# Performance work log

Hardware: AMD Instinct MI355X
Metric: run time of the kernel (lower is better)

The kernel has to match this reference:

```python
import jax, jax.numpy as jnp
import numpy as np

K = 7          # window kernel size
PAD = 3        # padding so out spatial == in spatial (stride=1, dilation=1)
BN_EPS = 1e-5


def conv1x1(x, w, b):
    # x: (b,c,h,w), w: (o,c), b: (o,)
    return jnp.einsum('bchw,oc->bohw', x, w) + b[None, :, None, None]


def bn_relu(x, bn):
    # bn: (4, C) rows = gamma, beta, running_mean, running_var (inference-mode BN)
    g, bta, m, v = bn[0], bn[1], bn[2], bn[3]
    scale = g / jnp.sqrt(v + BN_EPS)
    y = (x - m[None, :, None, None]) * scale[None, :, None, None] + bta[None, :, None, None]
    return jax.nn.relu(y)


def extract_patches(x):
    # Equivalent of F.unfold(x, K, padding=PAD, stride=1) reshaped to (b, C, K*K, H, W).
    # Ordering matches torch: channel major, kernel positions row-major.
    b, c, h, w = x.shape
    xp = jnp.pad(x, ((0, 0), (0, 0), (PAD, PAD), (PAD, PAD)))
    ps = [xp[:, :, i:i + h, j:j + w] for i in range(K) for j in range(K)]
    return jnp.stack(ps, axis=2)  # (b, c, K*K, h, w)


def setup_inputs() -> dict:
    key = jax.random.key(0)
    ks = jax.random.split(key, 20)
    Cin, Ck, Cv, Co = 256, 64, 128, 256
    b, h, w = 2, 96, 96

    def wgt(k, o, c):
        return jax.random.normal(k, (o, c), jnp.float32) * 0.05

    def bias(k, o):
        return jax.random.normal(k, (o,), jnp.float32) * 0.02

    def bn(k, c):
        g = 1.0 + 0.1 * jax.random.normal(k, (c,), jnp.float32)
        bta = 0.1 * jax.random.normal(jax.random.fold_in(k, 1), (c,), jnp.float32)
        m = 0.05 * jax.random.normal(jax.random.fold_in(k, 2), (c,), jnp.float32)
        v = 1.0 + 0.1 * jax.random.uniform(jax.random.fold_in(k, 3), (c,), jnp.float32)
        return jnp.stack([g, bta, m, v])  # (4, c)

    return {
        'x': jax.random.normal(ks[0], (b, Cin, h, w), jnp.float32),
        'fk_w1': wgt(ks[1], Ck, Cin), 'fk_b1': bias(ks[2], Ck), 'fk_bn1': bn(ks[3], Ck),
        'fk_w2': wgt(ks[4], Ck, Ck), 'fk_b2': bias(ks[5], Ck), 'fk_bn2': bn(ks[6], Ck),
        'fq_w1': wgt(ks[7], Ck, Cin), 'fq_b1': bias(ks[8], Ck), 'fq_bn1': bn(ks[9], Ck),
        'fq_w2': wgt(ks[10], Ck, Ck), 'fq_b2': bias(ks[11], Ck), 'fq_bn2': bn(ks[12], Ck),
        'fv_w': wgt(ks[13], Cv, Cin), 'fv_b': bias(ks[14], Cv),
        'W_w': wgt(ks[15], Co, Cv), 'W_b': bias(ks[16], Co),
    }


def reference(x, fk_w1, fk_b1, fk_bn1, fk_w2, fk_b2, fk_bn2,
              fq_w1, fq_b1, fq_bn1, fq_w2, fq_b2, fq_bn2,
              fv_w, fv_b, W_w, W_b):
    # scale=1 -> no pooling. stride=1, dilation=1, pad=3, k=7 -> out spatial == in spatial.
    value = conv1x1(x, fv_w, fv_b)                       # (b, Cv, H, W)
    unfold_value = extract_patches(value)                # (b, Cv, 49, H, W)

    k1 = bn_relu(conv1x1(x, fk_w1, fk_b1), fk_bn1)
    key = bn_relu(conv1x1(k1, fk_w2, fk_b2), fk_bn2)     # (b, Ck, H, W)
    unfold_key = extract_patches(key)                    # (b, Ck, 49, H, W)

    q1 = bn_relu(conv1x1(x, fq_w1, fq_b1), fq_bn1)
    query = bn_relu(conv1x1(q1, fq_w2, fq_b2), fq_bn2)   # (b, Ck, H, W)
    # start_index = dilation*(k//2) - padding = 0; stride=1 -> query slice is identity.

    sim = jnp.sum(unfold_key * query[:, :, None], axis=1, keepdims=True)  # (b,1,49,H,W)
    sim = jax.nn.softmax(sim, axis=2)
    context = jnp.sum(sim * unfold_value, axis=2)        # (b, Cv, H, W)
    context = conv1x1(context, W_w, W_b)                 # (b, Co, H, W)
    # F.interpolate to (h, w) with align_corners=True is identity (same size).
    return context
```

## Files before the change

kernel.cpp:

```cpp
#include <hip/hip_runtime.h>
#include <hip/hip_bf16.h>

typedef _Float16 f16;
typedef _Float16 f16x8 __attribute__((ext_vector_type(8)));
typedef float f32x4 __attribute__((ext_vector_type(4)));

#define HH 96
#define WW 96
#define HWs 9216
#define BN_EPS 1e-5f

#define OFF_XT   0u
#define OFF_ACT1 9437184u
#define OFF_ACT2 18874368u
#define OFF_CTX  23592960u
#define OFF_W1   28311552u
#define OFF_W2   28442624u
#define OFF_W3   28459008u
#define OFF_ST   28524544u

__global__ __launch_bounds__(256) void prep_kernel(
    const float* __restrict__ fk_w1, const float* __restrict__ fk_b1, const float* __restrict__ fk_bn1,
    const float* __restrict__ fk_w2, const float* __restrict__ fk_b2, const float* __restrict__ fk_bn2,
    const float* __restrict__ fq_w1, const float* __restrict__ fq_b1, const float* __restrict__ fq_bn1,
    const float* __restrict__ fq_w2, const float* __restrict__ fq_b2, const float* __restrict__ fq_bn2,
    const float* __restrict__ fv_w,  const float* __restrict__ fv_b,
    const float* __restrict__ W_w,   const float* __restrict__ W_b,
    char* __restrict__ wsb)
{
  f16* w1 = (f16*)(wsb + OFF_W1);
  f16* w2 = (f16*)(wsb + OFF_W2);
  f16* w3 = (f16*)(wsb + OFF_W3);
  float* st = (float*)(wsb + OFF_ST);
  int i = blockIdx.x * 256 + threadIdx.x;
  if (i < 65536) {
    int o = i >> 8, c = i & 255;
    float v;
    if (o < 128)      v = fv_w[o * 256 + c];
    else if (o < 192) v = fk_w1[(o - 128) * 256 + c];
    else              v = fq_w1[(o - 192) * 256 + c];
    w1[i] = (f16)v;
  } else if (i < 73728) {
    int j = i - 65536; int o = j >> 6, c = j & 63;
    w2[j] = (f16)((o < 64) ? fk_w2[o * 64 + c] : fq_w2[(o - 64) * 64 + c]);
  } else if (i < 106496) {
    int j = i - 73728;
    w3[j] = (f16)W_w[j];
  } else if (i < 106752) {
    int o = i - 106496;
    float s, t;
    if (o < 128) { s = 1.0f; t = fv_b[o]; }
    else if (o < 192) {
      int j = o - 128;
      float g = fk_bn1[j], be = fk_bn1[64 + j], m = fk_bn1[128 + j], v = fk_bn1[192 + j];
      s = g * rsqrtf(v + BN_EPS); t = (fk_b1[j] - m) * s + be;
    } else {
      int j = o - 192;
      float g = fq_bn1[j], be = fq_bn1[64 + j], m = fq_bn1[128 + j], v = fq_bn1[192 + j];
      s = g * rsqrtf(v + BN_EPS); t = (fq_b1[j] - m) * s + be;
    }
    st[o] = s; st[256 + o] = t;
  } else if (i < 106880) {
    int o = i - 106752;
    float s, t;
    if (o < 64) {
      float g = fk_bn2[o], be = fk_bn2[64 + o], m = fk_bn2[128 + o], v = fk_bn2[192 + o];
      s = g * rsqrtf(v + BN_EPS); t = (fk_b2[o] - m) * s + be;
    } else {
      int j = o - 64;
      float g = fq_bn2[j], be = fq_bn2[64 + j], m = fq_bn2[128 + j], v = fq_bn2[192 + j];
      s = g * rsqrtf(v + BN_EPS); t = (fq_b2[j] - m) * s + be;
    }
    st[512 + o] = s; st[640 + o] = t;
  } else if (i < 107136) {
    int o = i - 106880;
    st[768 + o] = W_b[o];
  }
}

__global__ __launch_bounds__(256) void transpose_in(const float* __restrict__ x, f16* __restrict__ xT)
{
  __shared__ float lds[64 * 65];
  const int t = threadIdx.x;
  const int p0 = blockIdx.x * 64, c0 = blockIdx.y * 64, bb = blockIdx.z;
#pragma unroll
  for (int pass = 0; pass < 16; ++pass) {
    int ch = pass * 4 + (t >> 6), px = t & 63;
    lds[ch * 65 + px] = x[((size_t)bb * 256 + c0 + ch) * HWs + p0 + px];
  }
  __syncthreads();
#pragma unroll
  for (int pass = 0; pass < 2; ++pass) {
    int pl = pass * 32 + (t >> 3), cs = t & 7;
    f16x8 v;
#pragma unroll
    for (int j = 0; j < 8; j++) v[j] = (f16)lds[(cs * 8 + j) * 65 + pl];
    *(f16x8*)&xT[((size_t)bb * HWs + p0 + pl) * 256 + c0 + cs * 8] = v;
  }
}

template<int KTOT, bool NCHW_OUT>
__global__ __launch_bounds__(256) void gemm128(
    const f16* __restrict__ Aact, int lda, int ka0,
    const f16* __restrict__ W,
    f16* __restrict__ Cout, int ldc, int cbase,
    float* __restrict__ out_nchw,
    const float* __restrict__ S, const float* __restrict__ T, int relu_start)
{
  __shared__ f16 As[128 * 40];
  __shared__ f16 Bs[128 * 40];
  const int tid = threadIdx.x;
  const int l = tid & 63, w = tid >> 6;
  const int bb = blockIdx.z;
  const int p0 = blockIdx.x * 128, n0 = blockIdx.y * 128;
  const f16* Ab = Aact + (size_t)bb * HWs * lda;
  f32x4 acc[4][4];
#pragma unroll
  for (int i = 0; i < 4; i++)
#pragma unroll
    for (int j = 0; j < 4; j++) acc[i][j] = (f32x4){0.f, 0.f, 0.f, 0.f};
  const int wm = (w >> 1) * 64, wn = (w & 1) * 64;
  const int lrow = l & 15, lk = (l >> 4) * 8;
#pragma unroll 1
  for (int ks = 0; ks < KTOT / 32; ks++) {
#pragma unroll
    for (int it = 0; it < 2; it++) {
      int tt = it * 256 + tid;
      int row = tt >> 2, seg = tt & 3;
      *(f16x8*)&As[row * 40 + seg * 8] =
          *(const f16x8*)&Ab[(size_t)(p0 + row) * lda + ka0 + ks * 32 + seg * 8];
      *(f16x8*)&Bs[row * 40 + seg * 8] =
          *(const f16x8*)&W[(size_t)(n0 + row) * KTOT + ks * 32 + seg * 8];
    }
    __syncthreads();
    f16x8 a[4], b[4];
#pragma unroll
    for (int mi = 0; mi < 4; mi++) a[mi] = *(const f16x8*)&As[(wm + mi * 16 + lrow) * 40 + lk];
#pragma unroll
    for (int ni = 0; ni < 4; ni++) b[ni] = *(const f16x8*)&Bs[(wn + ni * 16 + lrow) * 40 + lk];
#pragma unroll
    for (int mi = 0; mi < 4; mi++)
#pragma unroll
      for (int ni = 0; ni < 4; ni++)
        acc[mi][ni] = __builtin_amdgcn_mfma_f32_16x16x32_f16(a[mi], b[ni], acc[mi][ni], 0, 0, 0);
    __syncthreads();
  }
#pragma unroll
  for (int mi = 0; mi < 4; mi++)
#pragma unroll
    for (int ni = 0; ni < 4; ni++) {
      int coutl = n0 + wn + ni * 16 + lrow;
      int pb = p0 + wm + mi * 16 + (l >> 4) * 4;
      if (NCHW_OUT) {
        float t = T[coutl];
        float4 o;
        o.x = acc[mi][ni][0] + t; o.y = acc[mi][ni][1] + t;
        o.z = acc[mi][ni][2] + t; o.w = acc[mi][ni][3] + t;
        *(float4*)&out_nchw[((size_t)bb * 256 + coutl) * HWs + pb] = o;
      } else {
        float s = S[coutl], t = T[coutl];
        bool rl = coutl >= relu_start;
#pragma unroll
        for (int r = 0; r < 4; r++) {
          float v = acc[mi][ni][r] * s + t;
          if (rl) v = fmaxf(v, 0.f);
          Cout[((size_t)bb * HWs + pb + r) * ldc + cbase + coutl] = (f16)v;
        }
      }
    }
}

__global__ __launch_bounds__(256) void gemm_s2(
    const f16* __restrict__ Aact, int ka0,
    const f16* __restrict__ W,
    f16* __restrict__ Cout, int cbase,
    const float* __restrict__ S, const float* __restrict__ T)
{
  __shared__ f16 As[256 * 40];
  __shared__ f16 Bs[64 * 40];
  const int tid = threadIdx.x;
  const int l = tid & 63, w = tid >> 6;
  const int bb = blockIdx.z;
  const int p0 = blockIdx.x * 256;
  const f16* Ab = Aact + (size_t)bb * HWs * 256;
  f32x4 acc[4][4];
#pragma unroll
  for (int i = 0; i < 4; i++)
#pragma unroll
    for (int j = 0; j < 4; j++) acc[i][j] = (f32x4){0.f, 0.f, 0.f, 0.f};
  const int wm = w * 64;
  const int lrow = l & 15, lk = (l >> 4) * 8;
#pragma unroll 1
  for (int ks = 0; ks < 2; ks++) {
#pragma unroll
    for (int it = 0; it < 4; it++) {
      int tt = it * 256 + tid;
      int row = tt >> 2, seg = tt & 3;
      *(f16x8*)&As[row * 40 + seg * 8] =
          *(const f16x8*)&Ab[(size_t)(p0 + row) * 256 + ka0 + ks * 32 + seg * 8];
    }
    {
      int row = tid >> 2, seg = tid & 3;
      *(f16x8*)&Bs[row * 40 + seg * 8] =
          *(const f16x8*)&W[(size_t)row * 64 + ks * 32 + seg * 8];
    }
    __syncthreads();
    f16x8 a[4], b[4];
#pragma unroll
    for (int mi = 0; mi < 4; mi++) a[mi] = *(const f16x8*)&As[(wm + mi * 16 + lrow) * 40 + lk];
#pragma unroll
    for (int ni = 0; ni < 4; ni++) b[ni] = *(const f16x8*)&Bs[(ni * 16 + lrow) * 40 + lk];
#pragma unroll
    for (int mi = 0; mi < 4; mi++)
#pragma unroll
      for (int ni = 0; ni < 4; ni++)
        acc[mi][ni] = __builtin_amdgcn_mfma_f32_16x16x32_f16(a[mi], b[ni], acc[mi][ni], 0, 0, 0);
    __syncthreads();
  }
#pragma unroll
  for (int mi = 0; mi < 4; mi++)
#pragma unroll
    for (int ni = 0; ni < 4; ni++) {
      int coutl = ni * 16 + lrow;
      int pb = p0 + wm + mi * 16 + (l >> 4) * 4;
      float s = S[coutl], t = T[coutl];
#pragma unroll
      for (int r = 0; r < 4; r++) {
        float v = fmaxf(acc[mi][ni][r] * s + t, 0.f);
        Cout[((size_t)bb * HWs + pb + r) * 128 + cbase + coutl] = (f16)v;
      }
    }
}

__global__ __launch_bounds__(256) void attn_kernel(const f16* __restrict__ act1,
                                                   const f16* __restrict__ act2,
                                                   f16* __restrict__ ctx)
{
  __shared__ float Ps[64 * 52];
  __shared__ f16 buf[208 * 136];
  const int tid = threadIdx.x;
  const int l = tid & 63, w = tid >> 6;
  const int bb = blockIdx.z;
  const int x0 = blockIdx.x * 8, y0 = blockIdx.y * 8;
  const f16* a2 = act2 + (size_t)bb * HWs * 128;
  const f16* a1 = act1 + (size_t)bb * HWs * 256;
  f16* ctxb = ctx + (size_t)bb * HWs * 128;
  f16* Qs = buf;
  f16* Ks = buf + 64 * 72;

#pragma unroll
  for (int it = 0; it < 2; it++) {
    int t = it * 256 + tid;
    int q = t >> 3, seg = t & 7;
    int gp = (y0 + (q >> 3)) * WW + x0 + (q & 7);
    *(f16x8*)&Qs[q * 72 + seg * 8] = *(const f16x8*)&a2[(size_t)gp * 128 + 64 + seg * 8];
  }
  for (int t = tid; t < 1664; t += 256) {
    int kk = t >> 3, seg = t & 7;
    int ky = (kk * 4682) >> 16, kx = kk - 14 * ky;
    int gy = y0 - 3 + ky, gx = x0 - 3 + kx;
    f16x8 v = {(f16)0, (f16)0, (f16)0, (f16)0, (f16)0, (f16)0, (f16)0, (f16)0};
    if (kk < 196 && (unsigned)gy < (unsigned)HH && (unsigned)gx < (unsigned)WW)
      v = *(const f16x8*)&a2[((size_t)(gy * WW + gx)) * 128 + seg * 8];
    *(f16x8*)&Ks[kk * 72 + seg * 8] = v;
  }
  __syncthreads();

  f32x4 sc[13];
#pragma unroll
  for (int nj = 0; nj < 13; nj++) sc[nj] = (f32x4){0.f, 0.f, 0.f, 0.f};
  const int lrow = l & 15, lk = (l >> 4) * 8;
#pragma unroll
  for (int ks = 0; ks < 2; ks++) {
    f16x8 aq = *(const f16x8*)&Qs[(w * 16 + lrow) * 72 + ks * 32 + lk];
#pragma unroll
    for (int nj = 0; nj < 13; nj++) {
      f16x8 bk = *(const f16x8*)&Ks[(nj * 16 + lrow) * 72 + ks * 32 + lk];
      sc[nj] = __builtin_amdgcn_mfma_f32_16x16x32_f16(aq, bk, sc[nj], 0, 0, 0);
    }
  }
  const int r0 = w * 16 + (l >> 4) * 4;
#pragma unroll
  for (int nj = 0; nj < 13; nj++) {
    int c = nj * 16 + lrow;
    int ky = (c * 4682) >> 16, kx = c - 14 * ky;
#pragma unroll
    for (int r = 0; r < 4; r++) {
      int qy = (r0 + r) >> 3, qx = (r0 + r) & 7;
      bool valid = ((unsigned)(ky - qy) < 7u) && ((unsigned)(kx - qx) < 7u);
      if (!valid) sc[nj][r] = -1e30f;
    }
  }
  float mx[4], sm[4], inv[4];
#pragma unroll
  for (int r = 0; r < 4; r++) {
    mx[r] = -1e30f;
#pragma unroll
    for (int nj = 0; nj < 13; nj++) mx[r] = fmaxf(mx[r], sc[nj][r]);
  }
#pragma unroll
  for (int off = 1; off < 16; off <<= 1)
#pragma unroll
    for (int r = 0; r < 4; r++) mx[r] = fmaxf(mx[r], __shfl_xor(mx[r], off));
#pragma unroll
  for (int r = 0; r < 4; r++) sm[r] = 0.f;
#pragma unroll
  for (int nj = 0; nj < 13; nj++)
#pragma unroll
    for (int r = 0; r < 4; r++) {
      float e = __expf(sc[nj][r] - mx[r]);
      sc[nj][r] = e; sm[r] += e;
    }
#pragma unroll
  for (int off = 1; off < 16; off <<= 1)
#pragma unroll
    for (int r = 0; r < 4; r++) sm[r] += __shfl_xor(sm[r], off);
#pragma unroll
  for (int r = 0; r < 4; r++) inv[r] = 1.0f / sm[r];
#pragma unroll
  for (int nj = 0; nj < 13; nj++) {
    int c = nj * 16 + lrow;
    int ky = (c * 4682) >> 16, kx = c - 14 * ky;
#pragma unroll
    for (int r = 0; r < 4; r++) {
      int qy = (r0 + r) >> 3, qx = (r0 + r) & 7;
      int dy = ky - qy, dx = kx - qx;
      if (((unsigned)dy < 7u) && ((unsigned)dx < 7u))
        Ps[(r0 + r) * 52 + dy * 7 + dx] = sc[nj][r] * inv[r];
    }
  }
  __syncthreads();

  f16* Vs = buf;
  for (int t = tid; t < 3328; t += 256) {
    int kk = t >> 4, seg = t & 15;
    int ky = (kk * 4682) >> 16, kx = kk - 14 * ky;
    int gy = y0 - 3 + ky, gx = x0 - 3 + kx;
    f16x8 v = {(f16)0, (f16)0, (f16)0, (f16)0, (f16)0, (f16)0, (f16)0, (f16)0};
    if (kk < 196 && (unsigned)gy < (unsigned)HH && (unsigned)gx < (unsigned)WW)
      v = *(const f16x8*)&a1[((size_t)(gy * WW + gx)) * 256 + seg * 8];
    *(f16x8*)&Vs[kk * 136 + seg * 8] = v;
  }
  __syncthreads();

  const int q = tid >> 2;
  const int qy = q >> 3, qx = q & 7;
  const int ch0 = (tid & 3) * 32;
  float acc[32];
#pragma unroll
  for (int i = 0; i < 32; i++) acc[i] = 0.f;
#pragma unroll
  for (int dy = 0; dy < 7; dy++)
#pragma unroll
    for (int dx = 0; dx < 7; dx++) {
      float p = Ps[q * 52 + dy * 7 + dx];
      int kk = (qy + dy) * 14 + qx + dx;
      const f16* vp = &Vs[kk * 136 + ch0];
#pragma unroll
      for (int s = 0; s < 4; s++) {
        f16x8 v = *(const f16x8*)&vp[s * 8];
#pragma unroll
        for (int j = 0; j < 8; j++) acc[s * 8 + j] += (float)v[j] * p;
      }
    }
  int gp = (y0 + qy) * WW + x0 + qx;
#pragma unroll
  for (int s = 0; s < 4; s++) {
    f16x8 o;
#pragma unroll
    for (int j = 0; j < 8; j++) o[j] = (f16)acc[s * 8 + j];
    *(f16x8*)&ctxb[(size_t)gp * 128 + ch0 + s * 8] = o;
  }
}

extern "C" void kernel_launch(void* const* d_in, const int* in_sizes, int n_in,
                              void* d_out, int out_size, void* d_ws, size_t ws_size,
                              hipStream_t stream) {
  (void)in_sizes; (void)n_in; (void)out_size; (void)ws_size;
  const float* x      = (const float*)d_in[0];
  const float* fk_w1  = (const float*)d_in[1];
  const float* fk_b1  = (const float*)d_in[2];
  const float* fk_bn1 = (const float*)d_in[3];
  const float* fk_w2  = (const float*)d_in[4];
  const float* fk_b2  = (const float*)d_in[5];
  const float* fk_bn2 = (const float*)d_in[6];
  const float* fq_w1  = (const float*)d_in[7];
  const float* fq_b1  = (const float*)d_in[8];
  const float* fq_bn1 = (const float*)d_in[9];
  const float* fq_w2  = (const float*)d_in[10];
  const float* fq_b2  = (const float*)d_in[11];
  const float* fq_bn2 = (const float*)d_in[12];
  const float* fv_w   = (const float*)d_in[13];
  const float* fv_b   = (const float*)d_in[14];
  const float* W_w    = (const float*)d_in[15];
  const float* W_b    = (const float*)d_in[16];
  char* wsb = (char*)d_ws;
  float* out = (float*)d_out;

  f16* xT   = (f16*)(wsb + OFF_XT);
  f16* act1 = (f16*)(wsb + OFF_ACT1);
  f16* act2 = (f16*)(wsb + OFF_ACT2);
  f16* ctx  = (f16*)(wsb + OFF_CTX);
  f16* w1   = (f16*)(wsb + OFF_W1);
  f16* w2   = (f16*)(wsb + OFF_W2);
  f16* w3   = (f16*)(wsb + OFF_W3);
  float* st = (float*)(wsb + OFF_ST);

  prep_kernel<<<dim3(419), dim3(256), 0, stream>>>(
      fk_w1, fk_b1, fk_bn1, fk_w2, fk_b2, fk_bn2,
      fq_w1, fq_b1, fq_bn1, fq_w2, fq_b2, fq_bn2, fv_w, fv_b, W_w, W_b, wsb);

  transpose_in<<<dim3(144, 4, 2), dim3(256), 0, stream>>>(x, xT);

  gemm128<256, false><<<dim3(72, 2, 2), dim3(256), 0, stream>>>(
      xT, 256, 0, w1, act1, 256, 0, nullptr, st, st + 256, 128);

  gemm_s2<<<dim3(36, 1, 2), dim3(256), 0, stream>>>(
      act1, 128, w2, act2, 0, st + 512, st + 640);
  gemm_s2<<<dim3(36, 1, 2), dim3(256), 0, stream>>>(
      act1, 192, w2 + 64 * 64, act2, 64, st + 512 + 64, st + 640 + 64);

  attn_kernel<<<dim3(12, 12, 2), dim3(256), 0, stream>>>(act1, act2, ctx);

  gemm128<128, true><<<dim3(72, 2, 2), dim3(256), 0, stream>>>(
      ctx, 128, 0, w3, nullptr, 0, 0, out, st, st + 768, 1 << 30);
}
```

Before: 158.3 us.

## Fuse input transpose and conv stages, and fold final 1x1 conv into attention

The separate transpose, first-stage GEMM and two second-stage GEMMs are merged into one conv12 kernel. It reads fp32 NCHW input directly, keeps key/query intermediates in shared memory and applies the second 1x1 conv per 32-pixel tile. The attention kernel now also runs the output projection from a shared-memory context tile and writes NCHW output, removing the ctx buffer round trip and four launches. The trade-offs are smaller GEMM tiles with W1 reloaded per block, strided uncoalesced x reads, and scattered 4-byte output stores.

Result: faster. 138.9 us, median of 2 (-12.2%).

```diff
diff --git a/kernel.cpp b/kernel.cpp
--- a/kernel.cpp
+++ b/kernel.cpp
@@ -2,6 +2,7 @@
 #include <hip/hip_bf16.h>
 
 typedef _Float16 f16;
+typedef _Float16 f16x4 __attribute__((ext_vector_type(4)));
 typedef _Float16 f16x8 __attribute__((ext_vector_type(8)));
 typedef float f32x4 __attribute__((ext_vector_type(4)));
 
@@ -10,14 +11,12 @@
 #define HWs 9216
 #define BN_EPS 1e-5f
 
-#define OFF_XT   0u
-#define OFF_ACT1 9437184u
-#define OFF_ACT2 18874368u
-#define OFF_CTX  23592960u
-#define OFF_W1   28311552u
-#define OFF_W2   28442624u
-#define OFF_W3   28459008u
-#define OFF_ST   28524544u
+#define OFF_ACT1 0u
+#define OFF_ACT2 4718592u
+#define OFF_W1   9437184u
+#define OFF_W2   9568256u
+#define OFF_W3   9584640u
+#define OFF_ST   9650176u
 
 __global__ __launch_bounds__(256) void prep_kernel(
     const float* __restrict__ fk_w1, const float* __restrict__ fk_b1, const float* __restrict__ fk_bn1,
@@ -78,163 +77,115 @@
   }
 }
 
-__global__ __launch_bounds__(256) void transpose_in(const float* __restrict__ x, f16* __restrict__ xT)
+__global__ __launch_bounds__(256) void conv12(
+    const float* __restrict__ x, const f16* __restrict__ W1, const f16* __restrict__ W2,
+    f16* __restrict__ act1, f16* __restrict__ act2, const float* __restrict__ st)
 {
-  __shared__ float lds[64 * 65];
-  const int t = threadIdx.x;
-  const int p0 = blockIdx.x * 64, c0 = blockIdx.y * 64, bb = blockIdx.z;
-#pragma unroll
-  for (int pass = 0; pass < 16; ++pass) {
-    int ch = pass * 4 + (t >> 6), px = t & 63;
-    lds[ch * 65 + px] = x[((size_t)bb * 256 + c0 + ch) * HWs + p0 + px];
-  }
-  __syncthreads();
-#pragma unroll
-  for (int pass = 0; pass < 2; ++pass) {
-    int pl = pass * 32 + (t >> 3), cs = t & 7;
-    f16x8 v;
-#pragma unroll
-    for (int j = 0; j < 8; j++) v[j] = (f16)lds[(cs * 8 + j) * 65 + pl];
-    *(f16x8*)&xT[((size_t)bb * HWs + p0 + pl) * 256 + c0 + cs * 8] = v;
-  }
-}
-
-template<int KTOT, bool NCHW_OUT>
-__global__ __launch_bounds__(256) void gemm128(
-    const f16* __restrict__ Aact, int lda, int ka0,
-    const f16* __restrict__ W,
-    f16* __restrict__ Cout, int ldc, int cbase,
-    float* __restrict__ out_nchw,
-    const float* __restrict__ S, const float* __restrict__ T, int relu_start)
-{
-  __shared__ f16 As[128 * 40];
-  __shared__ f16 Bs[128 * 40];
+  __shared__ f16 As[32 * 40];
+  __shared__ f16 Bs[256 * 40];
+  __shared__ f16 kqs[2][32 * 72];
   const int tid = threadIdx.x;
   const int l = tid & 63, w = tid >> 6;
-  const int bb = blockIdx.z;
-  const int p0 = blockIdx.x * 128, n0 = blockIdx.y * 128;
-  const f16* Ab = Aact + (size_t)bb * HWs * lda;
-  f32x4 acc[4][4];
-#pragma unroll
-  for (int i = 0; i < 4; i++)
+  const int bb = blockIdx.y;
+  const int p0 = blockIdx.x * 32;
+  const int lrow = l & 15, lk = (l >> 4) * 8;
+
+  f32x4 acc[2][4];
+#pragma unroll
+  for (int i = 0; i < 2; i++)
 #pragma unroll
     for (int j = 0; j < 4; j++) acc[i][j] = (f32x4){0.f, 0.f, 0.f, 0.f};
-  const int wm = (w >> 1) * 64, wn = (w & 1) * 64;
-  const int lrow = l & 15, lk = (l >> 4) * 8;
+
+  const int spx = tid & 31, skg = tid >> 5;
 #pragma unroll 1
-  for (int ks = 0; ks < KTOT / 32; ks++) {
-#pragma unroll
-    for (int it = 0; it < 2; it++) {
-      int tt = it * 256 + tid;
-      int row = tt >> 2, seg = tt & 3;
-      *(f16x8*)&As[row * 40 + seg * 8] =
-          *(const f16x8*)&Ab[(size_t)(p0 + row) * lda + ka0 + ks * 32 + seg * 8];
-      *(f16x8*)&Bs[row * 40 + seg * 8] =
-          *(const f16x8*)&W[(size_t)(n0 + row) * KTOT + ks * 32 + seg * 8];
-    }
-    __syncthreads();
-    f16x8 a[4], b[4];
-#pragma unroll
-    for (int mi = 0; mi < 4; mi++) a[mi] = *(const f16x8*)&As[(wm + mi * 16 + lrow) * 40 + lk];
-#pragma unroll
-    for (int ni = 0; ni < 4; ni++) b[ni] = *(const f16x8*)&Bs[(wn + ni * 16 + lrow) * 40 + lk];
-#pragma unroll
-    for (int mi = 0; mi < 4; mi++)
-#pragma unroll
-      for (int ni = 0; ni < 4; ni++)
-        acc[mi][ni] = __builtin_amdgcn_mfma_f32_16x16x32_f16(a[mi], b[ni], acc[mi][ni], 0, 0, 0);
-    __syncthreads();
-  }
-#pragma unroll
-  for (int mi = 0; mi < 4; mi++)
-#pragma unroll
-    for (int ni = 0; ni < 4; ni++) {
-      int coutl = n0 + wn + ni * 16 + lrow;
-      int pb = p0 + wm + mi * 16 + (l >> 4) * 4;
-      if (NCHW_OUT) {
-        float t = T[coutl];
-        float4 o;
-        o.x = acc[mi][ni][0] + t; o.y = acc[mi][ni][1] + t;
-        o.z = acc[mi][ni][2] + t; o.w = acc[mi][ni][3] + t;
-        *(float4*)&out_nchw[((size_t)bb * 256 + coutl) * HWs + pb] = o;
-      } else {
-        float s = S[coutl], t = T[coutl];
-        bool rl = coutl >= relu_start;
-#pragma unroll
-        for (int r = 0; r < 4; r++) {
-          float v = acc[mi][ni][r] * s + t;
-          if (rl) v = fmaxf(v, 0.f);
-          Cout[((size_t)bb * HWs + pb + r) * ldc + cbase + coutl] = (f16)v;
-        }
-      }
-    }
-}
-
-__global__ __launch_bounds__(256) void gemm_s2(
-    const f16* __restrict__ Aact, int ka0,
-    const f16* __restrict__ W,
-    f16* __restrict__ Cout, int cbase,
-    const float* __restrict__ S, const float* __restrict__ T)
-{
-  __shared__ f16 As[256 * 40];
-  __shared__ f16 Bs[64 * 40];
-  const int tid = threadIdx.x;
-  const int l = tid & 63, w = tid >> 6;
-  const int bb = blockIdx.z;
-  const int p0 = blockIdx.x * 256;
-  const f16* Ab = Aact + (size_t)bb * HWs * 256;
-  f32x4 acc[4][4];
-#pragma unroll
-  for (int i = 0; i < 4; i++)
-#pragma unroll
-    for (int j = 0; j < 4; j++) acc[i][j] = (f32x4){0.f, 0.f, 0.f, 0.f};
-  const int wm = w * 64;
-  const int lrow = l & 15, lk = (l >> 4) * 8;
-#pragma unroll 1
-  for (int ks = 0; ks < 2; ks++) {
+  for (int ks = 0; ks < 8; ks++) {
+    f16x4 av;
+#pragma unroll
+    for (int j = 0; j < 4; j++)
+      av[j] = (f16)x[((size_t)bb * 256 + ks * 32 + skg * 4 + j) * HWs + p0 + spx];
+    *(f16x4*)&As[spx * 40 + skg * 4] = av;
 #pragma unroll
     for (int it = 0; it < 4; it++) {
       int tt = it * 256 + tid;
       int row = tt >> 2, seg = tt & 3;
-      *(f16x8*)&As[row * 40 + seg * 8] =
-          *(const f16x8*)&Ab[(size_t)(p0 + row) * 256 + ka0 + ks * 32 + seg * 8];
-    }
-    {
-      int row = tid >> 2, seg = tid & 3;
       *(f16x8*)&Bs[row * 40 + seg * 8] =
-          *(const f16x8*)&W[(size_t)row * 64 + ks * 32 + seg * 8];
+          *(const f16x8*)&W1[(size_t)row * 256 + ks * 32 + seg * 8];
     }
     __syncthreads();
-    f16x8 a[4], b[4];
-#pragma unroll
-    for (int mi = 0; mi < 4; mi++) a[mi] = *(const f16x8*)&As[(wm + mi * 16 + lrow) * 40 + lk];
-#pragma unroll
-    for (int ni = 0; ni < 4; ni++) b[ni] = *(const f16x8*)&Bs[(ni * 16 + lrow) * 40 + lk];
-#pragma unroll
-    for (int mi = 0; mi < 4; mi++)
-#pragma unroll
-      for (int ni = 0; ni < 4; ni++)
-        acc[mi][ni] = __builtin_amdgcn_mfma_f32_16x16x32_f16(a[mi], b[ni], acc[mi][ni], 0, 0, 0);
+    f16x8 a[2], b[4];
+#pragma unroll
+    for (int mi = 0; mi < 2; mi++) a[mi] = *(const f16x8*)&As[(mi * 16 + lrow) * 40 + lk];
+#pragma unroll
+    for (int nj = 0; nj < 4; nj++) b[nj] = *(const f16x8*)&Bs[(w * 64 + nj * 16 + lrow) * 40 + lk];
+#pragma unroll
+    for (int mi = 0; mi < 2; mi++)
+#pragma unroll
+      for (int nj = 0; nj < 4; nj++)
+        acc[mi][nj] = __builtin_amdgcn_mfma_f32_16x16x32_f16(a[mi], b[nj], acc[mi][nj], 0, 0, 0);
     __syncthreads();
   }
-#pragma unroll
-  for (int mi = 0; mi < 4; mi++)
-#pragma unroll
-    for (int ni = 0; ni < 4; ni++) {
-      int coutl = ni * 16 + lrow;
-      int pb = p0 + wm + mi * 16 + (l >> 4) * 4;
-      float s = S[coutl], t = T[coutl];
+
+#pragma unroll
+  for (int mi = 0; mi < 2; mi++)
+#pragma unroll
+    for (int nj = 0; nj < 4; nj++) {
+      int cout = w * 64 + nj * 16 + lrow;
+      float s = st[cout], t = st[256 + cout];
 #pragma unroll
       for (int r = 0; r < 4; r++) {
-        float v = fmaxf(acc[mi][ni][r] * s + t, 0.f);
-        Cout[((size_t)bb * HWs + pb + r) * 128 + cbase + coutl] = (f16)v;
+        int px = mi * 16 + (l >> 4) * 4 + r;
+        float v = acc[mi][nj][r] * s + t;
+        if (w < 2) {
+          act1[((size_t)bb * HWs + p0 + px) * 128 + cout] = (f16)v;
+        } else {
+          kqs[w - 2][px * 72 + (nj * 16 + lrow)] = (f16)fmaxf(v, 0.f);
+        }
       }
     }
+  __syncthreads();
+
+  const int sel = w >> 1, half = w & 1;
+  const f16* W2s = W2 + sel * 64 * 64;
+  f32x4 acc2[2][2];
+#pragma unroll
+  for (int i = 0; i < 2; i++)
+#pragma unroll
+    for (int j = 0; j < 2; j++) acc2[i][j] = (f32x4){0.f, 0.f, 0.f, 0.f};
+#pragma unroll
+  for (int ks = 0; ks < 2; ks++) {
+    f16x8 a2[2], b2[2];
+#pragma unroll
+    for (int mi = 0; mi < 2; mi++)
+      a2[mi] = *(const f16x8*)&kqs[sel][(mi * 16 + lrow) * 72 + ks * 32 + lk];
+#pragma unroll
+    for (int nj = 0; nj < 2; nj++)
+      b2[nj] = *(const f16x8*)&W2s[(size_t)(half * 32 + nj * 16 + lrow) * 64 + ks * 32 + lk];
+#pragma unroll
+    for (int mi = 0; mi < 2; mi++)
+#pragma unroll
+      for (int nj = 0; nj < 2; nj++)
+        acc2[mi][nj] = __builtin_amdgcn_mfma_f32_16x16x32_f16(a2[mi], b2[nj], acc2[mi][nj], 0, 0, 0);
+  }
+#pragma unroll
+  for (int mi = 0; mi < 2; mi++)
+#pragma unroll
+    for (int nj = 0; nj < 2; nj++) {
+      int c2 = sel * 64 + half * 32 + nj * 16 + lrow;
+      float s = st[512 + c2], t = st[640 + c2];
+#pragma unroll
+      for (int r = 0; r < 4; r++) {
+        int px = mi * 16 + (l >> 4) * 4 + r;
+        float v = fmaxf(acc2[mi][nj][r] * s + t, 0.f);
+        act2[((size_t)bb * HWs + p0 + px) * 128 + c2] = (f16)v;
+      }
+    }
 }
 
-__global__ __launch_bounds__(256) void attn_kernel(const f16* __restrict__ act1,
-                                                   const f16* __restrict__ act2,
-                                                   f16* __restrict__ ctx)
+__global__ __launch_bounds__(256) void attn_final(const f16* __restrict__ act1,
+                                                  const f16* __restrict__ act2,
+                                                  const f16* __restrict__ W3,
+                                                  const float* __restrict__ st,
+                                                  float* __restrict__ out)
 {
   __shared__ float Ps[64 * 52];
   __shared__ f16 buf[208 * 136];
@@ -243,10 +194,10 @@
   const int bb = blockIdx.z;
   const int x0 = blockIdx.x * 8, y0 = blockIdx.y * 8;
   const f16* a2 = act2 + (size_t)bb * HWs * 128;
-  const f16* a1 = act1 + (size_t)bb * HWs * 256;
-  f16* ctxb = ctx + (size_t)bb * HWs * 128;
+  const f16* a1 = act1 + (size_t)bb * HWs * 128;
   f16* Qs = buf;
   f16* Ks = buf + 64 * 72;
+  const int lrow = l & 15, lk = (l >> 4) * 8;
 
 #pragma unroll
   for (int it = 0; it < 2; it++) {
@@ -269,7 +220,6 @@
   f32x4 sc[13];
 #pragma unroll
   for (int nj = 0; nj < 13; nj++) sc[nj] = (f32x4){0.f, 0.f, 0.f, 0.f};
-  const int lrow = l & 15, lk = (l >> 4) * 8;
 #pragma unroll
   for (int ks = 0; ks < 2; ks++) {
     f16x8 aq = *(const f16x8*)&Qs[(w * 16 + lrow) * 72 + ks * 32 + lk];
@@ -338,7 +288,7 @@
     int gy = y0 - 3 + ky, gx = x0 - 3 + kx;
     f16x8 v = {(f16)0, (f16)0, (f16)0, (f16)0, (f16)0, (f16)0, (f16)0, (f16)0};
     if (kk < 196 && (unsigned)gy < (unsigned)HH && (unsigned)gx < (unsigned)WW)
-      v = *(const f16x8*)&a1[((size_t)(gy * WW + gx)) * 256 + seg * 8];
+      v = *(const f16x8*)&a1[((size_t)(gy * WW + gx)) * 128 + seg * 8];
     *(f16x8*)&Vs[kk * 136 + seg * 8] = v;
   }
   __syncthreads();
@@ -363,14 +313,50 @@
         for (int j = 0; j < 8; j++) acc[s * 8 + j] += (float)v[j] * p;
       }
     }
-  int gp = (y0 + qy) * WW + x0 + qx;
+  __syncthreads();
+
+  f16* ctxs = buf;
 #pragma unroll
   for (int s = 0; s < 4; s++) {
     f16x8 o;
 #pragma unroll
     for (int j = 0; j < 8; j++) o[j] = (f16)acc[s * 8 + j];
-    *(f16x8*)&ctxb[(size_t)gp * 128 + ch0 + s * 8] = o;
-  }
+    *(f16x8*)&ctxs[q * 136 + ch0 + s * 8] = o;
+  }
+  __syncthreads();
+
+  f32x4 fac[4][4];
+#pragma unroll
+  for (int i = 0; i < 4; i++)
+#pragma unroll
+    for (int j = 0; j < 4; j++) fac[i][j] = (f32x4){0.f, 0.f, 0.f, 0.f};
+#pragma unroll
+  for (int ks = 0; ks < 4; ks++) {
+    f16x8 a3[4], b3[4];
+#pragma unroll
+    for (int mi = 0; mi < 4; mi++)
+      a3[mi] = *(const f16x8*)&W3[(size_t)(w * 64 + mi * 16 + lrow) * 128 + ks * 32 + lk];
+#pragma unroll
+    for (int nj = 0; nj < 4; nj++)
+      b3[nj] = *(const f16x8*)&ctxs[(nj * 16 + lrow) * 136 + ks * 32 + lk];
+#pragma unroll
+    for (int mi = 0; mi < 4; mi++)
+#pragma unroll
+      for (int nj = 0; nj < 4; nj++)
+        fac[mi][nj] = __builtin_amdgcn_mfma_f32_16x16x32_f16(a3[mi], b3[nj], fac[mi][nj], 0, 0, 0);
+  }
+#pragma unroll
+  for (int mi = 0; mi < 4; mi++)
+#pragma unroll
+    for (int nj = 0; nj < 4; nj++) {
+#pragma unroll
+      for (int r = 0; r < 4; r++) {
+        int cout = w * 64 + mi * 16 + (l >> 4) * 4 + r;
+        int px = nj * 16 + lrow;
+        int gp = (y0 + (px >> 3)) * WW + x0 + (px & 7);
+        out[((size_t)bb * 256 + cout) * HWs + gp] = fac[mi][nj][r] + st[768 + cout];
+      }
+    }
 }
 
 extern "C" void kernel_launch(void* const* d_in, const int* in_sizes, int n_in,
@@ -397,10 +383,8 @@
   char* wsb = (char*)d_ws;
   float* out = (float*)d_out;
 
-  f16* xT   = (f16*)(wsb + OFF_XT);
   f16* act1 = (f16*)(wsb + OFF_ACT1);
   f16* act2 = (f16*)(wsb + OFF_ACT2);
-  f16* ctx  = (f16*)(wsb + OFF_CTX);
   f16* w1   = (f16*)(wsb + OFF_W1);
   f16* w2   = (f16*)(wsb + OFF_W2);
   f16* w3   = (f16*)(wsb + OFF_W3);
@@ -410,18 +394,7 @@
       fk_w1, fk_b1, fk_bn1, fk_w2, fk_b2, fk_bn2,
       fq_w1, fq_b1, fq_bn1, fq_w2, fq_b2, fq_bn2, fv_w, fv_b, W_w, W_b, wsb);
 
-  transpose_in<<<dim3(144, 4, 2), dim3(256), 0, stream>>>(x, xT);
-
-  gemm128<256, false><<<dim3(72, 2, 2), dim3(256), 0, stream>>>(
-      xT, 256, 0, w1, act1, 256, 0, nullptr, st, st + 256, 128);
-
-  gemm_s2<<<dim3(36, 1, 2), dim3(256), 0, stream>>>(
-      act1, 128, w2, act2, 0, st + 512, st + 640);
-  gemm_s2<<<dim3(36, 1, 2), dim3(256), 0, stream>>>(
-      act1, 192, w2 + 64 * 64, act2, 64, st + 512 + 64, st + 640 + 64);
-
-  attn_kernel<<<dim3(12, 12, 2), dim3(256), 0, stream>>>(act1, act2, ctx);
-
-  gemm128<128, true><<<dim3(72, 2, 2), dim3(256), 0, stream>>>(
-      ctx, 128, 0, w3, nullptr, 0, 0, out, st, st + 768, 1 << 30);
+  conv12<<<dim3(288, 2), dim3(256), 0, stream>>>(x, w1, w2, act1, act2, st);
+
+  attn_final<<<dim3(12, 12, 2), dim3(256), 0, stream>>>(act1, act2, w3, st, out);
 }
```
